# Kernel optimization log

Hardware: AMD Instinct MI355X
Metric: run time of the kernel (lower is better)

Reference implementation:

```python
import jax, jax.numpy as jnp
import numpy as np

N = 8192
E = 524288
D_IN, D_HID, D_OUT = 3, 16, 16


def setup_inputs() -> dict:
    key = jax.random.key(0)
    ks = jax.random.split(key, 9)
    node_feats = jax.random.normal(ks[0], (N, D_IN), dtype=jnp.float32)
    edge_idx = jax.random.randint(ks[1], (2, E), 0, N, dtype=jnp.int64)
    # GIN epsilon (train_eps=True -> learned scalar, init 0)
    eps = jnp.zeros((), dtype=jnp.float32)
    # MLP params (Kaiming-uniform-ish scale)
    def lin(k, fan_in, fan_out):
        lim = 1.0 / np.sqrt(fan_in)
        kw, kb = jax.random.split(k)
        W = jax.random.uniform(kw, (fan_in, fan_out), minval=-lim, maxval=lim, dtype=jnp.float32)
        b = jax.random.uniform(kb, (fan_out,), minval=-lim, maxval=lim, dtype=jnp.float32)
        return W, b
    W1, b1 = lin(ks[2], D_IN, D_HID)
    W2, b2 = lin(ks[3], D_HID, D_OUT)
    W3, b3 = lin(ks[4], D_OUT, 1)
    return {"node_feats": node_feats, "edge_idx": edge_idx, "eps": eps,
            "W1": W1, "b1": b1, "W2": W2, "b2": b2, "W3": W3, "b3": b3}


def reference(node_feats, edge_idx, eps, W1, b1, W2, b2, W3, b3):
    src, dst = edge_idx[0], edge_idx[1]
    # GIN aggregation: sum over incoming neighbor features (scatter-add at dst)
    agg = jax.ops.segment_sum(node_feats[src], dst, num_segments=N)  # [N, D_IN]
    z = (1.0 + eps) * node_feats + agg
    # 3-layer MLP with ReLU after every Linear
    h = jax.nn.relu(z @ W1 + b1)
    h = jax.nn.relu(h @ W2 + b2)
    h = jax.nn.relu(h @ W3 + b3)  # [N, 1]
    # outer product: [N,1] @ [1,N] -> [N,N]
    edge_feats = h @ h.T
    return edge_feats
```

## Files before the change

kernel.cpp:

```cpp
#include <hip/hip_runtime.h>
#include <hip/hip_bf16.h>

#define NN 8192
#define EE 524288
#define D_IN 3
#define D_HID 16
#define D_OUT 16
#define NAGG (NN * D_IN)
#define NAGG4 (NAGG / 4)
#define SLICES 64
#define QSPLIT 4
#define EPS_SLICE (EE / SLICES)
#define NODES_Q (NN / QSPLIT)
#define LELE (NODES_Q * D_IN)
#define ROWS_PER_BLK 4
#define NPB 64
#define C4B (NPB * D_IN / 4)
#define RCHUNK 4

typedef float f32x4 __attribute__((ext_vector_type(4)));

__device__ __forceinline__ float mlp_eval(float z0, float z1, float z2,
        const float* __restrict__ W1, const float* __restrict__ b1,
        const float* __restrict__ W2, const float* __restrict__ b2,
        const float* __restrict__ W3, const float* __restrict__ b3) {
    float h1[D_HID];
#pragma unroll
    for (int j = 0; j < D_HID; ++j) {
        float v = b1[j] + z0 * W1[0 * D_HID + j] + z1 * W1[1 * D_HID + j] + z2 * W1[2 * D_HID + j];
        h1[j] = v > 0.0f ? v : 0.0f;
    }
    float h2[D_OUT];
#pragma unroll
    for (int j = 0; j < D_OUT; ++j) {
        float v = b2[j];
#pragma unroll
        for (int k = 0; k < D_HID; ++k) v += h1[k] * W2[k * D_OUT + j];
        h2[j] = v > 0.0f ? v : 0.0f;
    }
    float v = b3[0];
#pragma unroll
    for (int k = 0; k < D_OUT; ++k) v += h2[k] * W3[k];
    return v > 0.0f ? v : 0.0f;
}

__global__ __launch_bounds__(512) void scatter_priv_kernel(
        const float* __restrict__ nf,
        const int* __restrict__ eidx,
        float* __restrict__ partials) {
    __shared__ float lagg[LELE];
    const int tid = threadIdx.x;
    const int slice = blockIdx.x & (SLICES - 1);
    const int q = blockIdx.x >> 6;
    for (int i = tid; i < LELE; i += 512) lagg[i] = 0.0f;
    __syncthreads();

    const int base = slice * EPS_SLICE;
    const int nlo = q * NODES_Q;
    for (int e = base + tid; e < base + EPS_SLICE; e += 512) {
        int d = eidx[EE + e];
        unsigned dq = (unsigned)(d - nlo);
        if (dq < (unsigned)NODES_Q) {
            int s = eidx[e];
            atomicAdd(&lagg[dq * 3 + 0], nf[s * 3 + 0]);
            atomicAdd(&lagg[dq * 3 + 1], nf[s * 3 + 1]);
            atomicAdd(&lagg[dq * 3 + 2], nf[s * 3 + 2]);
        }
    }
    __syncthreads();

    f32x4* __restrict__ dst = (f32x4*)(partials + (size_t)slice * NAGG + (size_t)nlo * D_IN);
    const f32x4* __restrict__ src = (const f32x4*)lagg;
    for (int i = tid; i < LELE / 4; i += 512) dst[i] = src[i];
}

__global__ __launch_bounds__(256) void reduce_mlp_fused_kernel(
        const float* __restrict__ partials,
        const float* __restrict__ nf,
        const float* __restrict__ epsp,
        const float* __restrict__ W1, const float* __restrict__ b1,
        const float* __restrict__ W2, const float* __restrict__ b2,
        const float* __restrict__ W3, const float* __restrict__ b3,
        float* __restrict__ h) {
    __shared__ f32x4 lq[C4B * RCHUNK];
    __shared__ f32x4 lz[C4B];
    const int t = threadIdx.x;
    if (t < C4B * RCHUNK) {
        const int q  = t / C4B;
        const int cl = t % C4B;
        const int c4 = blockIdx.x * C4B + cl;
        const f32x4* __restrict__ p = (const f32x4*)partials;
        f32x4 s = {0.0f, 0.0f, 0.0f, 0.0f};
#pragma unroll
        for (int k = 0; k < SLICES / RCHUNK; ++k)
            s += p[(size_t)(q * (SLICES / RCHUNK) + k) * NAGG4 + c4];
        lq[cl * RCHUNK + q] = s;
    }
    __syncthreads();
    if (t < C4B) {
        lz[t] = lq[t * RCHUNK + 0] + lq[t * RCHUNK + 1] +
                lq[t * RCHUNK + 2] + lq[t * RCHUNK + 3];
    }
    __syncthreads();

    if (t < NPB) {
        const int node = blockIdx.x * NPB + t;
        const float* __restrict__ l = (const float*)lz;
        const float eps1 = 1.0f + epsp[0];
        float z0 = eps1 * nf[node * 3 + 0] + l[t * 3 + 0];
        float z1 = eps1 * nf[node * 3 + 1] + l[t * 3 + 1];
        float z2 = eps1 * nf[node * 3 + 2] + l[t * 3 + 2];
        h[node] = mlp_eval(z0, z1, z2, W1, b1, W2, b2, W3, b3);
    }
}

__global__ void zero_agg_kernel(float* __restrict__ agg, int n) {
    int i = blockIdx.x * blockDim.x + threadIdx.x;
    if (i < n) agg[i] = 0.0f;
}

__global__ void scatter_atomic_kernel(const float* __restrict__ nf,
                                      const int* __restrict__ eidx,
                                      float* __restrict__ agg) {
    int e = blockIdx.x * blockDim.x + threadIdx.x;
    if (e >= EE) return;
    int s = eidx[e];
    int d = eidx[EE + e];
    atomicAdd(&agg[d * 3 + 0], nf[s * 3 + 0]);
    atomicAdd(&agg[d * 3 + 1], nf[s * 3 + 1]);
    atomicAdd(&agg[d * 3 + 2], nf[s * 3 + 2]);
}

__global__ void mlp_kernel(const float* __restrict__ nf,
                           const float* __restrict__ agg,
                           const float* __restrict__ epsp,
                           const float* __restrict__ W1, const float* __restrict__ b1,
                           const float* __restrict__ W2, const float* __restrict__ b2,
                           const float* __restrict__ W3, const float* __restrict__ b3,
                           float* __restrict__ h) {
    int i = blockIdx.x * blockDim.x + threadIdx.x;
    if (i >= NN) return;
    float eps1 = 1.0f + epsp[0];
    float z0 = eps1 * nf[i * 3 + 0] + agg[i * 3 + 0];
    float z1 = eps1 * nf[i * 3 + 1] + agg[i * 3 + 1];
    float z2 = eps1 * nf[i * 3 + 2] + agg[i * 3 + 2];
    h[i] = mlp_eval(z0, z1, z2, W1, b1, W2, b2, W3, b3);
}

__global__ __launch_bounds__(256) void outer_kernel(const float* __restrict__ h,
                                                    f32x4* __restrict__ out) {
    const int r0 = blockIdx.x * ROWS_PER_BLK;
    const float hi0 = h[r0 + 0];
    const float hi1 = h[r0 + 1];
    const float hi2 = h[r0 + 2];
    const float hi3 = h[r0 + 3];
    const f32x4* __restrict__ h4 = (const f32x4*)h;
    f32x4* __restrict__ row0 = out + (size_t)r0 * (NN / 4);
    f32x4* __restrict__ row1 = row0 + (NN / 4);
    f32x4* __restrict__ row2 = row1 + (NN / 4);
    f32x4* __restrict__ row3 = row2 + (NN / 4);
#pragma unroll 8
    for (int j = threadIdx.x; j < NN / 4; j += 256) {
        f32x4 v = h4[j];
        row0[j] = v * hi0;
        row1[j] = v * hi1;
        row2[j] = v * hi2;
        row3[j] = v * hi3;
    }
}

extern "C" void kernel_launch(void* const* d_in, const int* in_sizes, int n_in,
                              void* d_out, int out_size, void* d_ws, size_t ws_size,
                              hipStream_t stream) {
    const float* nf   = (const float*)d_in[0];
    const int*   eidx = (const int*)d_in[1];
    const float* eps  = (const float*)d_in[2];
    const float* W1   = (const float*)d_in[3];
    const float* b1   = (const float*)d_in[4];
    const float* W2   = (const float*)d_in[5];
    const float* b2   = (const float*)d_in[6];
    const float* W3   = (const float*)d_in[7];
    const float* b3   = (const float*)d_in[8];
    float* out = (float*)d_out;

    float* h        = (float*)d_ws;
    float* agg      = h + NN;
    float* partials = agg + NAGG;

    size_t need = (size_t)(NN + NAGG + (size_t)SLICES * NAGG) * sizeof(float);

    if (ws_size >= need) {
        scatter_priv_kernel<<<SLICES * QSPLIT, 512, 0, stream>>>(nf, eidx, partials);
        reduce_mlp_fused_kernel<<<NN / NPB, 256, 0, stream>>>(
            partials, nf, eps, W1, b1, W2, b2, W3, b3, h);
    } else {
        zero_agg_kernel<<<(NAGG + 255) / 256, 256, 0, stream>>>(agg, NAGG);
        scatter_atomic_kernel<<<(EE + 255) / 256, 256, 0, stream>>>(nf, eidx, agg);
        mlp_kernel<<<(NN + 255) / 256, 256, 0, stream>>>(nf, agg, eps, W1, b1, W2, b2, W3, b3, h);
    }
    outer_kernel<<<NN / ROWS_PER_BLK, 256, 0, stream>>>(h, (f32x4*)out);
}
```

Baseline: 66.38 us.

## Fuse partial reduction and MLP into scatter kernel via last-block counter

Replaces the separate reduce+MLP kernel with a last-block-done pattern: each scatter block bumps a per-quarter atomic counter, and the final block for each node quarter sums all 64 partials and evaluates the MLP. This removes one kernel launch and the inter-kernel gap, but adds a memset launch. The tail reduction now runs on only 4 blocks, each serially summing 64 slices for 2048 nodes, which reduces parallelism. There is also no explicit fence before the counter increment beyond the acq_rel atomic.

After: 106.1 us. 59.9% more time.

```diff
diff --git a/kernel.cpp b/kernel.cpp
--- a/kernel.cpp
+++ b/kernel.cpp
@@ -13,10 +13,8 @@
 #define EPS_SLICE (EE / SLICES)
 #define NODES_Q (NN / QSPLIT)
 #define LELE (NODES_Q * D_IN)
+#define C4Q (NODES_Q * D_IN / 4)
 #define ROWS_PER_BLK 4
-#define NPB 64
-#define C4B (NPB * D_IN / 4)
-#define RCHUNK 4
 
 typedef float f32x4 __attribute__((ext_vector_type(4)));
 
@@ -44,11 +42,18 @@
     return v > 0.0f ? v : 0.0f;
 }
 
-__global__ __launch_bounds__(512) void scatter_priv_kernel(
+__global__ __launch_bounds__(512) void scatter_reduce_kernel(
         const float* __restrict__ nf,
         const int* __restrict__ eidx,
-        float* __restrict__ partials) {
+        const float* __restrict__ epsp,
+        const float* __restrict__ W1, const float* __restrict__ b1,
+        const float* __restrict__ W2, const float* __restrict__ b2,
+        const float* __restrict__ W3, const float* __restrict__ b3,
+        float* __restrict__ partials,
+        int* __restrict__ cnt,
+        float* __restrict__ h) {
     __shared__ float lagg[LELE];
+    __shared__ int s_last;
     const int tid = threadIdx.x;
     const int slice = blockIdx.x & (SLICES - 1);
     const int q = blockIdx.x >> 6;
@@ -72,44 +77,39 @@
     f32x4* __restrict__ dst = (f32x4*)(partials + (size_t)slice * NAGG + (size_t)nlo * D_IN);
     const f32x4* __restrict__ src = (const f32x4*)lagg;
     for (int i = tid; i < LELE / 4; i += 512) dst[i] = src[i];
-}
-
-__global__ __launch_bounds__(256) void reduce_mlp_fused_kernel(
-        const float* __restrict__ partials,
-        const float* __restrict__ nf,
-        const float* __restrict__ epsp,
-        const float* __restrict__ W1, const float* __restrict__ b1,
-        const float* __restrict__ W2, const float* __restrict__ b2,
-        const float* __restrict__ W3, const float* __restrict__ b3,
-        float* __restrict__ h) {
-    __shared__ f32x4 lq[C4B * RCHUNK];
-    __shared__ f32x4 lz[C4B];
-    const int t = threadIdx.x;
-    if (t < C4B * RCHUNK) {
-        const int q  = t / C4B;
-        const int cl = t % C4B;
-        const int c4 = blockIdx.x * C4B + cl;
-        const f32x4* __restrict__ p = (const f32x4*)partials;
+    __syncthreads();
+
+    if (tid == 0) {
+        int old = __hip_atomic_fetch_add(&cnt[q], 1, __ATOMIC_ACQ_REL,
+                                         __HIP_MEMORY_SCOPE_AGENT);
+        s_last = (old == SLICES - 1);
+    }
+    __syncthreads();
+    if (!s_last) return;
+
+    f32x4* __restrict__ lz4 = (f32x4*)lagg;
+    const f32x4* __restrict__ p = (const f32x4*)partials;
+#pragma unroll
+    for (int pass = 0; pass < 3; ++pass) {
+        const int cl = pass * 512 + tid;
+        const int c4 = q * C4Q + cl;
         f32x4 s = {0.0f, 0.0f, 0.0f, 0.0f};
-#pragma unroll
-        for (int k = 0; k < SLICES / RCHUNK; ++k)
-            s += p[(size_t)(q * (SLICES / RCHUNK) + k) * NAGG4 + c4];
-        lq[cl * RCHUNK + q] = s;
-    }
-    __syncthreads();
-    if (t < C4B) {
-        lz[t] = lq[t * RCHUNK + 0] + lq[t * RCHUNK + 1] +
-                lq[t * RCHUNK + 2] + lq[t * RCHUNK + 3];
-    }
-    __syncthreads();
-
-    if (t < NPB) {
-        const int node = blockIdx.x * NPB + t;
-        const float* __restrict__ l = (const float*)lz;
-        const float eps1 = 1.0f + epsp[0];
-        float z0 = eps1 * nf[node * 3 + 0] + l[t * 3 + 0];
-        float z1 = eps1 * nf[node * 3 + 1] + l[t * 3 + 1];
-        float z2 = eps1 * nf[node * 3 + 2] + l[t * 3 + 2];
+#pragma unroll 8
+        for (int k = 0; k < SLICES; ++k)
+            s += p[(size_t)k * NAGG4 + c4];
+        lz4[cl] = s;
+    }
+    __syncthreads();
+
+    const float* __restrict__ l = (const float*)lz4;
+    const float eps1 = 1.0f + epsp[0];
+#pragma unroll
+    for (int u = 0; u < NODES_Q / 512; ++u) {
+        const int nl = u * 512 + tid;
+        const int node = q * NODES_Q + nl;
+        float z0 = eps1 * nf[node * 3 + 0] + l[nl * 3 + 0];
+        float z1 = eps1 * nf[node * 3 + 1] + l[nl * 3 + 1];
+        float z2 = eps1 * nf[node * 3 + 2] + l[nl * 3 + 2];
         h[node] = mlp_eval(z0, z1, z2, W1, b1, W2, b2, W3, b3);
     }
 }
@@ -186,13 +186,15 @@
     float* h        = (float*)d_ws;
     float* agg      = h + NN;
     float* partials = agg + NAGG;
-
-    size_t need = (size_t)(NN + NAGG + (size_t)SLICES * NAGG) * sizeof(float);
+    int*   cnt      = (int*)(partials + (size_t)SLICES * NAGG);
+
+    size_t need = (size_t)(NN + NAGG + (size_t)SLICES * NAGG) * sizeof(float)
+                  + QSPLIT * sizeof(int);
 
     if (ws_size >= need) {
-        scatter_priv_kernel<<<SLICES * QSPLIT, 512, 0, stream>>>(nf, eidx, partials);
-        reduce_mlp_fused_kernel<<<NN / NPB, 256, 0, stream>>>(
-            partials, nf, eps, W1, b1, W2, b2, W3, b3, h);
+        hipMemsetAsync(cnt, 0, QSPLIT * sizeof(int), stream);
+        scatter_reduce_kernel<<<SLICES * QSPLIT, 512, 0, stream>>>(
+            nf, eidx, eps, W1, b1, W2, b2, W3, b3, partials, cnt, h);
     } else {
         zero_agg_kernel<<<(NAGG + 255) / 256, 256, 0, stream>>>(agg, NAGG);
         scatter_atomic_kernel<<<(EE + 255) / 256, 256, 0, stream>>>(nf, eidx, agg);
```
